# Performance work log

Measured on AMD Instinct MI355X. Metric: run time of the kernel, lower is better.

The kernel has to match this reference:

```python
import jax, jax.numpy as jnp
import numpy as np

NUM_EMB = 200_000
DIM = 64
COMPRESSION = 0.25
UPDATE_COUNT = 2
HASHED_SIZE = int(NUM_EMB * DIM * COMPRESSION)  # 3,200,000
NUM_BAGS = 16384
BAG_LEN = 50
TOTAL = NUM_BAGS * BAG_LEN  # 819,200


def setup_inputs() -> dict:
    key = jax.random.key(0)
    k1, k2, k3 = jax.random.split(key, 3)
    # flat indices into the (virtual) [NUM_EMB, DIM] embedding table
    x = jax.random.randint(k1, (TOTAL,), 0, NUM_EMB, dtype=jnp.int32)
    # bag start offsets (equal-size bags of BAG_LEN)
    offsets = jnp.arange(NUM_BAGS, dtype=jnp.int32) * BAG_LEN
    # compressed parameter vector, init U(-sqrt(1/N), sqrt(1/N)) as in the module
    bound = float(np.sqrt(1.0 / NUM_EMB))
    hashed_weight = jax.random.uniform(k2, (HASHED_SIZE,), jnp.float32, -bound, bound)
    # hash index matrices: UPDATE_COUNT tables of shape [NUM_EMB, DIM],
    # values uniform in [0, HASHED_SIZE) (stands in for xxh32(i_j_idxU) % hN)
    weight_idx = jax.random.randint(k3, (UPDATE_COUNT, NUM_EMB, DIM), 0, HASHED_SIZE, dtype=jnp.int32)
    return {"x": x, "offsets": offsets, "hashed_weight": hashed_weight, "weight_idx": weight_idx}


def reference(x, offsets, hashed_weight, weight_idx):
    # Instead of materializing the full dense [NUM_EMB, DIM] table per update
    # (what F.embedding_bag(x, hashed_weight[idx]) does), gather only the rows
    # that x touches: same math, less traffic.
    per_idx = weight_idx[:, x, :]            # [U, T, D] int
    vals = hashed_weight[per_idx]            # [U, T, D]
    tok = vals.sum(axis=0)                   # sum over update_count -> [T, D]
    # embedding_bag 'sum' pooling via segment_sum over bags defined by offsets
    num_bags = offsets.shape[0]
    pos = jnp.arange(x.shape[0], dtype=offsets.dtype)
    seg = jnp.searchsorted(offsets, pos, side='right') - 1  # [T] bag id
    return jax.ops.segment_sum(tok, seg, num_segments=num_bags)  # [B, D]
```

## Files before the change

kernel.cpp:

```cpp
#include <hip/hip_runtime.h>
#include <hip/hip_fp16.h>

#define DIM 64
#define K_PASSES 8
#define EPT 8

typedef int          vint4   __attribute__((ext_vector_type(4)));
typedef float        vfloat4 __attribute__((ext_vector_type(4)));
typedef unsigned int vuint4  __attribute__((ext_vector_type(4)));

static __device__ __forceinline__ float2 h2f2(unsigned u) {
    __half2 h = __builtin_bit_cast(__half2, u);
    return __half22float2(h);
}

__global__ void emb_sum_kernel(const int* __restrict__ widx,
                               const float* __restrict__ hw,
                               __half* __restrict__ esum,
                               long long total ,
                               int hashed_size) {
    long long base = ((long long)blockIdx.x * blockDim.x + threadIdx.x) * EPT;
    if (base >= total) return;
    if (base + EPT <= total) {
        const vint4* w0 = (const vint4*)(widx + base);
        const vint4* w1 = (const vint4*)(widx + base + total);
        vint4 a0 = __builtin_nontemporal_load(w0);
        vint4 a1 = __builtin_nontemporal_load(w0 + 1);
        vint4 b0 = __builtin_nontemporal_load(w1);
        vint4 b1 = __builtin_nontemporal_load(w1 + 1);
        int idx[16] = {a0.x, a0.y, a0.z, a0.w, a1.x, a1.y, a1.z, a1.w,
                       b0.x, b0.y, b0.z, b0.w, b1.x, b1.y, b1.z, b1.w};
        float r[16];
#pragma unroll
        for (int i = 0; i < 16; ++i) r[i] = 0.0f;

        int slice = (hashed_size + K_PASSES - 1) / K_PASSES;
        int lo = 0;
        for (int k = 0; k < K_PASSES; ++k, lo += slice) {
#pragma unroll
            for (int i = 0; i < 16; ++i) {
                if ((unsigned)(idx[i] - lo) < (unsigned)slice)
                    r[i] += hw[idx[i]];
            }
        }
        unsigned u[4];
#pragma unroll
        for (int p = 0; p < 4; ++p) {
            float s0 = r[2 * p] + r[8 + 2 * p];
            float s1 = r[2 * p + 1] + r[8 + 2 * p + 1];
            __half2 h = __halves2half2(__float2half_rn(s0), __float2half_rn(s1));
            u[p] = __builtin_bit_cast(unsigned, h);
        }
        vuint4 o0 = {u[0], u[1], u[2], u[3]};
        __builtin_nontemporal_store(o0, (vuint4*)(esum + base));
    } else {
        for (long long g = base; g < total; ++g)
            esum[g] = __float2half_rn(hw[widx[g]] + hw[widx[g + total]]);
    }
}

__global__ void __launch_bounds__(256, 8)
bag_sum_kernel(const int* __restrict__ x,
               const int* __restrict__ offsets,
               const __half* __restrict__ esum,
               float* __restrict__ out,
               int num_bags, int total_tokens) {
    int wave = (int)((blockIdx.x * blockDim.x + threadIdx.x) >> 6);
    int lane = threadIdx.x & 63;
    if (wave >= num_bags) return;
    int group = lane >> 3;
    int l8    = lane & 7;
    int start = offsets[wave];
    int end = (wave + 1 < num_bags) ? offsets[wave + 1] : total_tokens;
    int n = end - start;

    float2 acc0 = {0.f, 0.f}, acc1 = {0.f, 0.f}, acc2 = {0.f, 0.f}, acc3 = {0.f, 0.f};

    if (n == 50) {
        int xv = (lane < 50) ? x[start + lane] : 0;
        int e[7];
#pragma unroll
        for (int j = 0; j < 7; ++j) {
            int src = j * 8 + group; if (src > 49) src = 49;
            e[j] = __shfl(xv, src, 64);
        }
        vuint4 v[7];
#pragma unroll
        for (int j = 0; j < 7; ++j)
            v[j] = ((const vuint4*)(esum + (size_t)e[j] * DIM))[l8];
#pragma unroll
        for (int j = 0; j < 7; ++j) {
            bool ok = (j < 6) || (group < 2);
            if (ok) {
                float2 f0 = h2f2(v[j].x), f1 = h2f2(v[j].y);
                float2 f2 = h2f2(v[j].z), f3 = h2f2(v[j].w);
                acc0.x += f0.x; acc0.y += f0.y;
                acc1.x += f1.x; acc1.y += f1.y;
                acc2.x += f2.x; acc2.y += f2.y;
                acc3.x += f3.x; acc3.y += f3.y;
            }
        }
    } else {
        for (int base = start; base < end; base += 64) {
            int nn = end - base;
            if (nn > 64) nn = 64;
            int xv = (lane < nn) ? x[base + lane] : 0;
            int i = 0;
#pragma unroll 2
            for (; i + 8 <= nn; i += 8) {
                int eo = __shfl(xv, i + group, 64);
                vuint4 v = ((const vuint4*)(esum + (size_t)eo * DIM))[l8];
                float2 f0 = h2f2(v.x), f1 = h2f2(v.y), f2 = h2f2(v.z), f3 = h2f2(v.w);
                acc0.x += f0.x; acc0.y += f0.y;
                acc1.x += f1.x; acc1.y += f1.y;
                acc2.x += f2.x; acc2.y += f2.y;
                acc3.x += f3.x; acc3.y += f3.y;
            }
            if (i < nn) {
                int r = nn - i;
                int src = i + group; if (src > nn - 1) src = nn - 1;
                int eo = __shfl(xv, src, 64);
                vuint4 v = ((const vuint4*)(esum + (size_t)eo * DIM))[l8];
                if (group < r) {
                    float2 f0 = h2f2(v.x), f1 = h2f2(v.y), f2 = h2f2(v.z), f3 = h2f2(v.w);
                    acc0.x += f0.x; acc0.y += f0.y;
                    acc1.x += f1.x; acc1.y += f1.y;
                    acc2.x += f2.x; acc2.y += f2.y;
                    acc3.x += f3.x; acc3.y += f3.y;
                }
            }
        }
    }

#pragma unroll
    for (int m = 8; m <= 32; m <<= 1) {
        acc0.x += __shfl_xor(acc0.x, m, 64); acc0.y += __shfl_xor(acc0.y, m, 64);
        acc1.x += __shfl_xor(acc1.x, m, 64); acc1.y += __shfl_xor(acc1.y, m, 64);
        acc2.x += __shfl_xor(acc2.x, m, 64); acc2.y += __shfl_xor(acc2.y, m, 64);
        acc3.x += __shfl_xor(acc3.x, m, 64); acc3.y += __shfl_xor(acc3.y, m, 64);
    }
    if (lane < 8) {
        vfloat4* orow = (vfloat4*)(out + (size_t)wave * DIM);
        vfloat4 p0 = {acc0.x, acc0.y, acc1.x, acc1.y};
        vfloat4 p1 = {acc2.x, acc2.y, acc3.x, acc3.y};
        orow[l8 * 2]     = p0;
        orow[l8 * 2 + 1] = p1;
    }
}

__global__ void direct_kernel(const int* __restrict__ x,
                              const int* __restrict__ offsets,
                              const float* __restrict__ hw,
                              const int* __restrict__ widx,
                              float* __restrict__ out,
                              int num_bags, int total_tokens,
                              long long emb_total) {
    int wave = (int)((blockIdx.x * blockDim.x + threadIdx.x) >> 6);
    int lane = threadIdx.x & 63;
    if (wave >= num_bags) return;
    int start = offsets[wave];
    int end = (wave + 1 < num_bags) ? offsets[wave + 1] : total_tokens;

    float acc = 0.0f;
    for (int t = start; t < end; ++t) {
        int e = x[t];
        const int* row = widx + (size_t)e * DIM;
        acc += hw[row[lane]] + hw[row[emb_total + lane]];
    }
    out[(size_t)wave * DIM + lane] = acc;
}

extern "C" void kernel_launch(void* const* d_in, const int* in_sizes, int n_in,
                              void* d_out, int out_size, void* d_ws, size_t ws_size,
                              hipStream_t stream) {
    const int*   x       = (const int*)d_in[0];
    const int*   offsets = (const int*)d_in[1];
    const float* hw      = (const float*)d_in[2];
    const int*   widx    = (const int*)d_in[3];
    float*       out     = (float*)d_out;

    int total_tokens = in_sizes[0];
    int num_bags     = in_sizes[1];
    int hashed_size  = in_sizes[2];
    long long widx_elems = in_sizes[3];
    long long emb_total  = widx_elems / 2;

    size_t need = (size_t)emb_total * sizeof(__half);

    if (ws_size >= need) {
        __half* esum = (__half*)d_ws;
        {
            long long nthreads = (emb_total + EPT - 1) / EPT;
            int block = 256;
            long long grid = (nthreads + block - 1) / block;
            emb_sum_kernel<<<(int)grid, block, 0, stream>>>(widx, hw, esum,
                                                            emb_total, hashed_size);
        }
        {
            int block = 256;
            int waves_per_block = block / 64;
            int grid = (num_bags + waves_per_block - 1) / waves_per_block;
            bag_sum_kernel<<<grid, block, 0, stream>>>(x, offsets, esum, out,
                                                       num_bags, total_tokens);
        }
    } else {
        int block = 256;
        int waves_per_block = block / 64;
        int grid = (num_bags + waves_per_block - 1) / waves_per_block;
        direct_kernel<<<grid, block, 0, stream>>>(x, offsets, hw, widx, out,
                                                  num_bags, total_tokens, emb_total);
    }
}
```

Measured before the change: 328.8 us.

## Replace per-bag gather with per-row binning and atomic scatter into bags

Adds a binning pass that uses atomic counters to record, for each embedding row, which bags reference it. A scatter pass then reads each used esum row once and adds it into every referencing bag's output with float atomics, and an overflow kernel handles rows referenced more than sixteen times. The aim is to stop re-reading esum rows once per token, at the cost of three memsets, extra launches, about 52M float atomics and a nondeterministic summation order. The old bag_sum kernel is kept as a fallback without its specialised length-50 path.

After: 547.0 us. 1.66x slower.

```diff
diff --git a/kernel.cpp b/kernel.cpp
--- a/kernel.cpp
+++ b/kernel.cpp
@@ -4,6 +4,8 @@
 #define DIM 64
 #define K_PASSES 8
 #define EPT 8
+#define BUCKET_CAP 16
+#define OVF_CAP 65536
 
 typedef int          vint4   __attribute__((ext_vector_type(4)));
 typedef float        vfloat4 __attribute__((ext_vector_type(4)));
@@ -17,8 +19,7 @@
 __global__ void emb_sum_kernel(const int* __restrict__ widx,
                                const float* __restrict__ hw,
                                __half* __restrict__ esum,
-                               long long total ,
-                               int hashed_size) {
+                               long long total, int hashed_size) {
     long long base = ((long long)blockIdx.x * blockDim.x + threadIdx.x) * EPT;
     if (base >= total) return;
     if (base + EPT <= total) {
@@ -33,7 +34,6 @@
         float r[16];
 #pragma unroll
         for (int i = 0; i < 16; ++i) r[i] = 0.0f;
-
         int slice = (hashed_size + K_PASSES - 1) / K_PASSES;
         int lo = 0;
         for (int k = 0; k < K_PASSES; ++k, lo += slice) {
@@ -56,6 +56,76 @@
     } else {
         for (long long g = base; g < total; ++g)
             esum[g] = __float2half_rn(hw[widx[g]] + hw[widx[g + total]]);
+    }
+}
+
+static __device__ __forceinline__ int bag_of(int t, const int* __restrict__ offsets,
+                                             int num_bags, int total_tokens) {
+    int avg = total_tokens / num_bags;
+    int b = t / avg;
+    if (b >= num_bags) b = num_bags - 1;
+    while (t < offsets[b]) --b;
+    while (b + 1 < num_bags && t >= offsets[b + 1]) ++b;
+    return b;
+}
+
+__global__ void bin_kernel(const int* __restrict__ x,
+                           const int* __restrict__ offsets,
+                           int* __restrict__ counts,
+                           int* __restrict__ buckets,
+                           int* __restrict__ ovf_cnt,
+                           int* __restrict__ ovf,
+                           int total_tokens, int num_bags) {
+    int t = blockIdx.x * blockDim.x + threadIdx.x;
+    if (t >= total_tokens) return;
+    int e = x[t];
+    int b = bag_of(t, offsets, num_bags, total_tokens);
+    int slot = atomicAdd(&counts[e], 1);
+    if (slot < BUCKET_CAP) {
+        buckets[(size_t)e * BUCKET_CAP + slot] = b;
+    } else {
+        int o = atomicAdd(ovf_cnt, 1);
+        if (o < OVF_CAP) ovf[o] = t;
+    }
+}
+
+__global__ void scatter_kernel(const __half* __restrict__ esum,
+                               const int* __restrict__ counts,
+                               const int* __restrict__ buckets,
+                               float* __restrict__ out,
+                               int num_emb) {
+    int wave = (int)((blockIdx.x * blockDim.x + threadIdx.x) >> 6);
+    int lane = threadIdx.x & 63;
+    if (wave >= num_emb) return;
+    int c = counts[wave];
+    if (c == 0) return;
+    if (c > BUCKET_CAP) c = BUCKET_CAP;
+    float v = __half2float(esum[(size_t)wave * DIM + lane]);
+    const int* bk = buckets + (size_t)wave * BUCKET_CAP;
+    for (int s = 0; s < c; ++s) {
+        int b = bk[s];
+        atomicAdd(out + (size_t)b * DIM + lane, v);
+    }
+}
+
+__global__ void overflow_kernel(const int* __restrict__ x,
+                                const int* __restrict__ offsets,
+                                const __half* __restrict__ esum,
+                                float* __restrict__ out,
+                                const int* __restrict__ ovf_cnt,
+                                const int* __restrict__ ovf,
+                                int total_tokens, int num_bags) {
+    int cnt = *ovf_cnt;
+    if (cnt > OVF_CAP) cnt = OVF_CAP;
+    int lane = threadIdx.x & 63;
+    int wave = (int)((blockIdx.x * blockDim.x + threadIdx.x) >> 6);
+    int nwaves = (gridDim.x * blockDim.x) >> 6;
+    for (int i = wave; i < cnt; i += nwaves) {
+        int t = ovf[i];
+        int e = x[t];
+        int b = bag_of(t, offsets, num_bags, total_tokens);
+        float v = __half2float(esum[(size_t)e * DIM + lane]);
+        atomicAdd(out + (size_t)b * DIM + lane, v);
     }
 }
 
@@ -68,70 +138,33 @@
     int wave = (int)((blockIdx.x * blockDim.x + threadIdx.x) >> 6);
     int lane = threadIdx.x & 63;
     if (wave >= num_bags) return;
-    int group = lane >> 3;
-    int l8    = lane & 7;
+    int group = lane >> 3, l8 = lane & 7;
     int start = offsets[wave];
     int end = (wave + 1 < num_bags) ? offsets[wave + 1] : total_tokens;
-    int n = end - start;
-
-    float2 acc0 = {0.f, 0.f}, acc1 = {0.f, 0.f}, acc2 = {0.f, 0.f}, acc3 = {0.f, 0.f};
-
-    if (n == 50) {
-        int xv = (lane < 50) ? x[start + lane] : 0;
-        int e[7];
-#pragma unroll
-        for (int j = 0; j < 7; ++j) {
-            int src = j * 8 + group; if (src > 49) src = 49;
-            e[j] = __shfl(xv, src, 64);
-        }
-        vuint4 v[7];
-#pragma unroll
-        for (int j = 0; j < 7; ++j)
-            v[j] = ((const vuint4*)(esum + (size_t)e[j] * DIM))[l8];
-#pragma unroll
-        for (int j = 0; j < 7; ++j) {
-            bool ok = (j < 6) || (group < 2);
-            if (ok) {
-                float2 f0 = h2f2(v[j].x), f1 = h2f2(v[j].y);
-                float2 f2 = h2f2(v[j].z), f3 = h2f2(v[j].w);
-                acc0.x += f0.x; acc0.y += f0.y;
-                acc1.x += f1.x; acc1.y += f1.y;
-                acc2.x += f2.x; acc2.y += f2.y;
-                acc3.x += f3.x; acc3.y += f3.y;
+    float2 acc0 = {0.f,0.f}, acc1 = {0.f,0.f}, acc2 = {0.f,0.f}, acc3 = {0.f,0.f};
+    for (int base = start; base < end; base += 64) {
+        int nn = end - base; if (nn > 64) nn = 64;
+        int xv = (lane < nn) ? x[base + lane] : 0;
+        int i = 0;
+        for (; i + 8 <= nn; i += 8) {
+            int eo = __shfl(xv, i + group, 64);
+            vuint4 v = ((const vuint4*)(esum + (size_t)eo * DIM))[l8];
+            float2 f0 = h2f2(v.x), f1 = h2f2(v.y), f2 = h2f2(v.z), f3 = h2f2(v.w);
+            acc0.x += f0.x; acc0.y += f0.y; acc1.x += f1.x; acc1.y += f1.y;
+            acc2.x += f2.x; acc2.y += f2.y; acc3.x += f3.x; acc3.y += f3.y;
+        }
+        if (i < nn) {
+            int r = nn - i;
+            int src = i + group; if (src > nn - 1) src = nn - 1;
+            int eo = __shfl(xv, src, 64);
+            vuint4 v = ((const vuint4*)(esum + (size_t)eo * DIM))[l8];
+            if (group < r) {
+                float2 f0 = h2f2(v.x), f1 = h2f2(v.y), f2 = h2f2(v.z), f3 = h2f2(v.w);
+                acc0.x += f0.x; acc0.y += f0.y; acc1.x += f1.x; acc1.y += f1.y;
+                acc2.x += f2.x; acc2.y += f2.y; acc3.x += f3.x; acc3.y += f3.y;
             }
         }
-    } else {
-        for (int base = start; base < end; base += 64) {
-            int nn = end - base;
-            if (nn > 64) nn = 64;
-            int xv = (lane < nn) ? x[base + lane] : 0;
-            int i = 0;
-#pragma unroll 2
-            for (; i + 8 <= nn; i += 8) {
-                int eo = __shfl(xv, i + group, 64);
-                vuint4 v = ((const vuint4*)(esum + (size_t)eo * DIM))[l8];
-                float2 f0 = h2f2(v.x), f1 = h2f2(v.y), f2 = h2f2(v.z), f3 = h2f2(v.w);
-                acc0.x += f0.x; acc0.y += f0.y;
-                acc1.x += f1.x; acc1.y += f1.y;
-                acc2.x += f2.x; acc2.y += f2.y;
-                acc3.x += f3.x; acc3.y += f3.y;
-            }
-            if (i < nn) {
-                int r = nn - i;
-                int src = i + group; if (src > nn - 1) src = nn - 1;
-                int eo = __shfl(xv, src, 64);
-                vuint4 v = ((const vuint4*)(esum + (size_t)eo * DIM))[l8];
-                if (group < r) {
-                    float2 f0 = h2f2(v.x), f1 = h2f2(v.y), f2 = h2f2(v.z), f3 = h2f2(v.w);
-                    acc0.x += f0.x; acc0.y += f0.y;
-                    acc1.x += f1.x; acc1.y += f1.y;
-                    acc2.x += f2.x; acc2.y += f2.y;
-                    acc3.x += f3.x; acc3.y += f3.y;
-                }
-            }
-        }
-    }
-
+    }
 #pragma unroll
     for (int m = 8; m <= 32; m <<= 1) {
         acc0.x += __shfl_xor(acc0.x, m, 64); acc0.y += __shfl_xor(acc0.y, m, 64);
@@ -143,8 +176,7 @@
         vfloat4* orow = (vfloat4*)(out + (size_t)wave * DIM);
         vfloat4 p0 = {acc0.x, acc0.y, acc1.x, acc1.y};
         vfloat4 p1 = {acc2.x, acc2.y, acc3.x, acc3.y};
-        orow[l8 * 2]     = p0;
-        orow[l8 * 2 + 1] = p1;
+        orow[l8 * 2] = p0; orow[l8 * 2 + 1] = p1;
     }
 }
 
@@ -153,14 +185,12 @@
                               const float* __restrict__ hw,
                               const int* __restrict__ widx,
                               float* __restrict__ out,
-                              int num_bags, int total_tokens,
-                              long long emb_total) {
+                              int num_bags, int total_tokens, long long emb_total) {
     int wave = (int)((blockIdx.x * blockDim.x + threadIdx.x) >> 6);
     int lane = threadIdx.x & 63;
     if (wave >= num_bags) return;
     int start = offsets[wave];
     int end = (wave + 1 < num_bags) ? offsets[wave + 1] : total_tokens;
-
     float acc = 0.0f;
     for (int t = start; t < end; ++t) {
         int e = x[t];
@@ -184,30 +214,64 @@
     int hashed_size  = in_sizes[2];
     long long widx_elems = in_sizes[3];
     long long emb_total  = widx_elems / 2;
-
-    size_t need = (size_t)emb_total * sizeof(__half);
-
-    if (ws_size >= need) {
-        __half* esum = (__half*)d_ws;
+    int num_emb = (int)(emb_total / DIM);
+
+    size_t esum_bytes   = (size_t)emb_total * sizeof(__half);
+    size_t counts_off   = (esum_bytes + 255) & ~(size_t)255;
+    size_t counts_bytes = (size_t)num_emb * sizeof(int);
+    size_t bucket_off   = (counts_off + counts_bytes + 255) & ~(size_t)255;
+    size_t bucket_bytes = (size_t)num_emb * BUCKET_CAP * sizeof(int);
+    size_t ovfc_off     = (bucket_off + bucket_bytes + 255) & ~(size_t)255;
+    size_t ovf_off      = ovfc_off + 256;
+    size_t need_full    = ovf_off + (size_t)OVF_CAP * sizeof(int);
+
+    char* ws = (char*)d_ws;
+
+    if (ws_size >= need_full) {
+        __half* esum   = (__half*)ws;
+        int*    counts = (int*)(ws + counts_off);
+        int*    bucket = (int*)(ws + bucket_off);
+        int*    ovfc   = (int*)(ws + ovfc_off);
+        int*    ovf    = (int*)(ws + ovf_off);
+
+        hipMemsetAsync(counts, 0, counts_bytes, stream);
+        hipMemsetAsync(ovfc, 0, sizeof(int), stream);
+        hipMemsetAsync(out, 0, (size_t)out_size * sizeof(float), stream);
+
         {
             long long nthreads = (emb_total + EPT - 1) / EPT;
-            int block = 256;
-            long long grid = (nthreads + block - 1) / block;
-            emb_sum_kernel<<<(int)grid, block, 0, stream>>>(widx, hw, esum,
-                                                            emb_total, hashed_size);
-        }
-        {
-            int block = 256;
-            int waves_per_block = block / 64;
-            int grid = (num_bags + waves_per_block - 1) / waves_per_block;
-            bag_sum_kernel<<<grid, block, 0, stream>>>(x, offsets, esum, out,
-                                                       num_bags, total_tokens);
+            long long grid = (nthreads + 255) / 256;
+            emb_sum_kernel<<<(int)grid, 256, 0, stream>>>(widx, hw, esum,
+                                                          emb_total, hashed_size);
+        }
+        {
+            int grid = (total_tokens + 255) / 256;
+            bin_kernel<<<grid, 256, 0, stream>>>(x, offsets, counts, bucket,
+                                                 ovfc, ovf, total_tokens, num_bags);
+        }
+        {
+            int waves_per_block = 4;
+            int grid = (num_emb + waves_per_block - 1) / waves_per_block;
+            scatter_kernel<<<grid, 256, 0, stream>>>(esum, counts, bucket, out, num_emb);
+        }
+        overflow_kernel<<<16, 256, 0, stream>>>(x, offsets, esum, out, ovfc, ovf,
+                                                total_tokens, num_bags);
+    } else if (ws_size >= esum_bytes) {
+        __half* esum = (__half*)ws;
+        {
+            long long nthreads = (emb_total + EPT - 1) / EPT;
+            long long grid = (nthreads + 255) / 256;
+            emb_sum_kernel<<<(int)grid, 256, 0, stream>>>(widx, hw, esum,
+                                                          emb_total, hashed_size);
+        }
+        {
+            int grid = (num_bags + 3) / 4;
+            bag_sum_kernel<<<grid, 256, 0, stream>>>(x, offsets, esum, out,
+                                                     num_bags, total_tokens);
         }
     } else {
-        int block = 256;
-        int waves_per_block = block / 64;
-        int grid = (num_bags + waves_per_block - 1) / waves_per_block;
-        direct_kernel<<<grid, block, 0, stream>>>(x, offsets, hw, widx, out,
-                                                  num_bags, total_tokens, emb_total);
-    }
-}
+        int grid = (num_bags + 3) / 4;
+        direct_kernel<<<grid, 256, 0, stream>>>(x, offsets, hw, widx, out,
+                                                num_bags, total_tokens, emb_total);
+    }
+}
```
